# Optimization experiments

Measured on AMD Instinct MI355X. Metric: run time of the kernel, lower is better.

## Reference

```python
import jax, jax.numpy as jnp
import numpy as np

N_NODES = 100000


def _gcn_norm(edge_index, num_nodes):
    # PyG gcn_norm with add_self_loops=True, symmetric normalization.
    src = jnp.concatenate([edge_index[0], jnp.arange(num_nodes)])
    dst = jnp.concatenate([edge_index[1], jnp.arange(num_nodes)])
    ones = jnp.ones(src.shape[0], dtype=jnp.float32)
    deg = jax.ops.segment_sum(ones, dst, num_segments=num_nodes)
    dinv = jnp.where(deg > 0, jax.lax.rsqrt(deg), 0.0)
    norm = dinv[src] * dinv[dst]  # [E + N]
    return src, dst, norm


def _gcn_conv(x, W, b, src, dst, norm, num_nodes):
    h = x @ W                                  # dense transform first (PyG order)
    msg = h[src] * norm[:, None]               # gather + scale, [E+N, D]
    agg = jax.ops.segment_sum(msg, dst, num_segments=num_nodes)
    return agg + b


def setup_inputs() -> dict:
    key = jax.random.key(0)
    ks = jax.random.split(key, 6)
    F_in, D, C, E = 256, 64, 47, 1200000
    x = jax.random.normal(ks[0], (N_NODES, F_in), dtype=jnp.float32)
    edge_index = jax.random.randint(ks[1], (2, E), 0, N_NODES)
    W1 = jax.random.normal(ks[2], (F_in, D), dtype=jnp.float32) * (1.0 / np.sqrt(F_in))
    b1 = jnp.zeros((D,), dtype=jnp.float32)
    W2 = jax.random.normal(ks[3], (D, C), dtype=jnp.float32) * (1.0 / np.sqrt(D))
    b2 = jnp.zeros((C,), dtype=jnp.float32)
    return {"x": x, "edge_index": edge_index, "W1": W1, "b1": b1, "W2": W2, "b2": b2}


def reference(x, edge_index, W1, b1, W2, b2):
    src, dst, norm = _gcn_norm(edge_index, N_NODES)
    h = jax.nn.relu(_gcn_conv(x, W1, b1, src, dst, norm, N_NODES))
    # dropout: eval mode (training=False) -> identity
    out = _gcn_conv(h, W2, b2, src, dst, norm, N_NODES)
    return jax.nn.log_softmax(out, axis=1)
```

## Files before the change

### kernel.cpp

```cpp
#include <hip/hip_runtime.h>
#include <math.h>

#define NN 100000
#define FIN 256
#define D1 64
#define C2 47
#define S2 48
#define PREPB 76
#define NBKT 391
#define CAP 4096

typedef unsigned short u16;
typedef unsigned int u32;
typedef __attribute__((ext_vector_type(8))) short short8;
typedef __attribute__((ext_vector_type(4))) float floatx4;

__device__ __forceinline__ u16 f2b(float f) {
    union { float f; unsigned u; } v; v.f = f;
    unsigned r = v.u + 0x7FFF + ((v.u >> 16) & 1);
    return (u16)(r >> 16);
}
__device__ __forceinline__ float b2f_lo(u32 p) { union { unsigned u; float f; } v; v.u = p << 16; return v.f; }
__device__ __forceinline__ float b2f_hi(u32 p) { union { unsigned u; float f; } v; v.u = p & 0xFFFF0000u; return v.f; }

__global__ __launch_bounds__(256) void k_prep_bucket(
    const float* __restrict__ W1, const float* __restrict__ W2,
    u16* __restrict__ W1t, u16* __restrict__ W2t,
    const int* __restrict__ src, const int* __restrict__ dst, int E,
    int* __restrict__ bucketCnt, u32* __restrict__ ebuf)
{
    int b = blockIdx.x;
    if (b < PREPB) {
        int i = b * 256 + threadIdx.x;
        if (i < FIN * D1) {
            int c = i >> 8, k = i & 255;
            W1t[i] = f2b(W1[k * D1 + c]);
        } else if (i < FIN * D1 + D1 * S2) {
            int j = i - FIN * D1;
            int c = j >> 6, k = j & 63;
            W2t[j] = (c < C2) ? f2b(W2[k * C2 + c]) : (u16)0;
        }
        return;
    }
    __shared__ int hist[NBKT];
    __shared__ int base[NBKT];
    const int t = threadIdx.x;
    const int blk = b - PREPB;
    for (int i = t; i < NBKT; i += 256) hist[i] = 0;
    __syncthreads();

    int e0 = blk * 2048 + t;
    u32 pk[8]; int bk[8], tk[8];
    #pragma unroll
    for (int j = 0; j < 8; ++j) {
        int e = e0 + j * 256;
        bk[j] = -1;
        if (e < E) {
            int d = dst[e];
            int s = src[e];
            bk[j] = d >> 8;
            pk[j] = (u32)s | ((u32)(d & 255) << 17);
            tk[j] = atomicAdd(&hist[bk[j]], 1);
        }
    }
    __syncthreads();
    for (int i = t; i < NBKT; i += 256)
        base[i] = hist[i] ? atomicAdd(&bucketCnt[i], hist[i]) : 0;
    __syncthreads();
    #pragma unroll
    for (int j = 0; j < 8; ++j)
        if (bk[j] >= 0)
            ebuf[(size_t)bk[j] * CAP + base[bk[j]] + tk[j]] = pk[j];
}

__global__ __launch_bounds__(256) void k_csr_ptr(const int* __restrict__ bucketCnt,
                                                 const u32* __restrict__ ebuf,
                                                 int* __restrict__ rowptr,
                                                 float* __restrict__ dinv, int E) {
    __shared__ int sd[256];
    __shared__ int hist[256];
    const int b = blockIdx.x, t = threadIdx.x;
    int v = ((t < b) ? bucketCnt[t] : 0) + ((t + 256 < b) ? bucketCnt[t + 256] : 0);
    sd[t] = v; __syncthreads();
    for (int off = 128; off; off >>= 1) {
        if (t < off) sd[t] += sd[t + off];
        __syncthreads();
    }
    int ebase = sd[0];
    __syncthreads();

    hist[t] = 0;
    __syncthreads();
    const int cnt = bucketCnt[b];
    const u32* eb = ebuf + (size_t)b * CAP;
    for (int i = t; i < cnt; i += 256)
        atomicAdd(&hist[eb[i] >> 17], 1);
    __syncthreads();

    int h = hist[t];
    sd[t] = h; __syncthreads();
    for (int off = 1; off < 256; off <<= 1) {
        int u = (t >= off) ? sd[t - off] : 0;
        __syncthreads();
        sd[t] += u;
        __syncthreads();
    }
    int node = b * 256 + t;
    if (node <= NN) rowptr[node] = ebase + sd[t] - h;
    if (node < NN) dinv[node] = rsqrtf((float)h + 1.0f);
}

__global__ __launch_bounds__(256) void k_fill_gemm1(
    const int* __restrict__ bucketCnt, const u32* __restrict__ ebuf,
    const int* __restrict__ rowptr, int* __restrict__ colidx,
    const float* __restrict__ x, const u16* __restrict__ W1t,
    const float* __restrict__ dinv, u16* __restrict__ hs1)
{
    int b = blockIdx.x;
    const int t = threadIdx.x;
    if (b < NBKT) {
        __shared__ int cur[256];
        int node = b * 256 + t;
        cur[t] = (node < NN) ? rowptr[node] : 0;
        __syncthreads();
        const int cnt = bucketCnt[b];
        const u32* eb = ebuf + (size_t)b * CAP;
        for (int i = t; i < cnt; i += 256) {
            u32 p = eb[i];
            int pos = atomicAdd(&cur[p >> 17], 1);
            colidx[pos] = p & 0x1FFFF;
        }
        return;
    }
    __shared__ short As[2][64 * 40];
    __shared__ short Bs[2][64 * 40];
    const int bm = (b - NBKT) * 64;
    const int w = t >> 6, lane = t & 63;
    const int arow = t >> 2;
    const int ak0 = (t & 3) * 8;

    floatx4 acc[4] = {};
    const int gr = bm + arow;
    const bool rowok = gr < NN;
    const float* xrow = x + (size_t)(rowok ? gr : 0) * FIN + ak0;

    float4 v0 = make_float4(0.f,0.f,0.f,0.f), v1 = v0;
    if (rowok) { v0 = *(const float4*)(xrow); v1 = *(const float4*)(xrow + 4); }
    short8 wv = *(const short8*)(W1t + arow * FIN + ak0);
    {
        short8 av;
        av[0]=(short)f2b(v0.x); av[1]=(short)f2b(v0.y); av[2]=(short)f2b(v0.z); av[3]=(short)f2b(v0.w);
        av[4]=(short)f2b(v1.x); av[5]=(short)f2b(v1.y); av[6]=(short)f2b(v1.z); av[7]=(short)f2b(v1.w);
        *(short8*)(&As[0][arow * 40 + ak0]) = av;
        *(short8*)(&Bs[0][arow * 40 + ak0]) = wv;
    }
    __syncthreads();

    int cb_ = 0;
    for (int kt = 32; kt <= FIN; kt += 32) {
        const bool more = kt < FIN;
        float4 n0, n1; short8 nw;
        if (more) {
            if (rowok) { n0 = *(const float4*)(xrow + kt); n1 = *(const float4*)(xrow + kt + 4); }
            else { n0 = make_float4(0.f,0.f,0.f,0.f); n1 = n0; }
            nw = *(const short8*)(W1t + arow * FIN + kt + ak0);
        }
        short8 af = *(const short8*)(&As[cb_][(w * 16 + (lane & 15)) * 40 + (lane >> 4) * 8]);
        #pragma unroll
        for (int cb = 0; cb < 4; ++cb) {
            short8 bv = *(const short8*)(&Bs[cb_][(cb * 16 + (lane & 15)) * 40 + (lane >> 4) * 8]);
            acc[cb] = __builtin_amdgcn_mfma_f32_16x16x32_bf16(af, bv, acc[cb], 0, 0, 0);
        }
        if (!more) break;
        short8 av;
        av[0]=(short)f2b(n0.x); av[1]=(short)f2b(n0.y); av[2]=(short)f2b(n0.z); av[3]=(short)f2b(n0.w);
        av[4]=(short)f2b(n1.x); av[5]=(short)f2b(n1.y); av[6]=(short)f2b(n1.z); av[7]=(short)f2b(n1.w);
        *(short8*)(&As[cb_ ^ 1][arow * 40 + ak0]) = av;
        *(short8*)(&Bs[cb_ ^ 1][arow * 40 + ak0]) = nw;
        __syncthreads();
        cb_ ^= 1;
    }

    #pragma unroll
    for (int cb = 0; cb < 4; ++cb) {
        #pragma unroll
        for (int r = 0; r < 4; ++r) {
            int grow = bm + w * 16 + (lane >> 4) * 4 + r;
            if (grow < NN) {
                float v = acc[cb][r] * dinv[grow];
                hs1[(size_t)grow * D1 + cb * 16 + (lane & 15)] = f2b(v);
            }
        }
    }
}

__global__ __launch_bounds__(256) void k_gather_gemm2(
    const int* __restrict__ rowptr, const int* __restrict__ colidx,
    const float* __restrict__ dinv, const u16* __restrict__ hs1,
    const float* __restrict__ b1, const u16* __restrict__ W2t,
    u16* __restrict__ hs2)
{
    __shared__ short As[2][64 * 40];
    __shared__ short Bs[2][48 * 40];
    const int t = threadIdx.x;
    const int bm = blockIdx.x * 64;
    const int w = t >> 6;
    const int l32 = t & 31;

    for (int s = t; s < 384; s += 256) {
        int kt = s / 192, rem = s - kt * 192;
        int r = rem >> 2, j = rem & 3;
        *(short8*)(&Bs[kt][r * 40 + j * 8]) =
            *(const short8*)(W2t + r * D1 + kt * 32 + j * 8);
    }

    {
        const int g = (t >> 5) & 1;
        float2 bb = *(const float2*)(b1 + 2 * l32);
        const int kth = l32 >> 4;
        const int cs  = (2 * l32) & 31;
        #pragma unroll 1
        for (int i = 0; i < 8; ++i) {
            int rl = w * 16 + g * 8 + i;
            int node = bm + rl;
            if (node >= NN) break;
            int beg = rowptr[node], end = rowptr[node + 1];
            u32 pv = *((const u32*)(hs1 + (size_t)node * D1) + l32);
            float a0 = b2f_lo(pv), b0 = b2f_hi(pv);
            float a1 = 0.f, b1v = 0.f, a2 = 0.f, b2v = 0.f, a3 = 0.f, b3v = 0.f;
            int e = beg;
            for (; e + 8 <= end; e += 8) {
                int s0 = colidx[e+0], s1 = colidx[e+1], s2 = colidx[e+2], s3 = colidx[e+3];
                int s4 = colidx[e+4], s5 = colidx[e+5], s6 = colidx[e+6], s7 = colidx[e+7];
                u32 p0 = *((const u32*)(hs1 + (size_t)s0 * D1) + l32);
                u32 p1 = *((const u32*)(hs1 + (size_t)s1 * D1) + l32);
                u32 p2 = *((const u32*)(hs1 + (size_t)s2 * D1) + l32);
                u32 p3 = *((const u32*)(hs1 + (size_t)s3 * D1) + l32);
                u32 p4 = *((const u32*)(hs1 + (size_t)s4 * D1) + l32);
                u32 p5 = *((const u32*)(hs1 + (size_t)s5 * D1) + l32);
                u32 p6 = *((const u32*)(hs1 + (size_t)s6 * D1) + l32);
                u32 p7 = *((const u32*)(hs1 + (size_t)s7 * D1) + l32);
                a0 += b2f_lo(p0); b0  += b2f_hi(p0);
                a1 += b2f_lo(p1); b1v += b2f_hi(p1);
                a2 += b2f_lo(p2); b2v += b2f_hi(p2);
                a3 += b2f_lo(p3); b3v += b2f_hi(p3);
                a0 += b2f_lo(p4); b0  += b2f_hi(p4);
                a1 += b2f_lo(p5); b1v += b2f_hi(p5);
                a2 += b2f_lo(p6); b2v += b2f_hi(p6);
                a3 += b2f_lo(p7); b3v += b2f_hi(p7);
            }
            for (; e + 4 <= end; e += 4) {
                int s0 = colidx[e+0], s1 = colidx[e+1], s2 = colidx[e+2], s3 = colidx[e+3];
                u32 p0 = *((const u32*)(hs1 + (size_t)s0 * D1) + l32);
                u32 p1 = *((const u32*)(hs1 + (size_t)s1 * D1) + l32);
                u32 p2 = *((const u32*)(hs1 + (size_t)s2 * D1) + l32);
                u32 p3 = *((const u32*)(hs1 + (size_t)s3 * D1) + l32);
                a0 += b2f_lo(p0); b0  += b2f_hi(p0);
                a1 += b2f_lo(p1); b1v += b2f_hi(p1);
                a2 += b2f_lo(p2); b2v += b2f_hi(p2);
                a3 += b2f_lo(p3); b3v += b2f_hi(p3);
            }
            for (; e < end; ++e) {
                u32 p0 = *((const u32*)(hs1 + (size_t)colidx[e] * D1) + l32);
                a0 += b2f_lo(p0); b0 += b2f_hi(p0);
            }
            float dd = dinv[node];
            float f0 = fmaxf(fmaf(dd, (a0 + a1) + (a2 + a3), bb.x), 0.f);
            float f1 = fmaxf(fmaf(dd, (b0 + b1v) + (b2v + b3v), bb.y), 0.f);
            u32 pk = (u32)f2b(f0) | ((u32)f2b(f1) << 16);
            *(u32*)(&As[kth][rl * 40 + cs]) = pk;
        }
    }
    __syncthreads();

    const int lane = t & 63;
    floatx4 acc[3] = {};
    #pragma unroll
    for (int kt = 0; kt < 2; ++kt) {
        short8 af = *(const short8*)(&As[kt][(w * 16 + (lane & 15)) * 40 + (lane >> 4) * 8]);
        #pragma unroll
        for (int cb = 0; cb < 3; ++cb) {
            short8 bv = *(const short8*)(&Bs[kt][(cb * 16 + (lane & 15)) * 40 + (lane >> 4) * 8]);
            acc[cb] = __builtin_amdgcn_mfma_f32_16x16x32_bf16(af, bv, acc[cb], 0, 0, 0);
        }
    }

    #pragma unroll
    for (int cb = 0; cb < 3; ++cb) {
        #pragma unroll
        for (int r = 0; r < 4; ++r) {
            int grow = bm + w * 16 + (lane >> 4) * 4 + r;
            if (grow < NN) {
                float v = acc[cb][r] * dinv[grow];
                hs2[(size_t)grow * S2 + cb * 16 + (lane & 15)] = f2b(v);
            }
        }
    }
}

__global__ __launch_bounds__(256) void k_gather47_sm(const int* __restrict__ rowptr,
                                                     const int* __restrict__ colidx,
                                                     const float* __restrict__ dinv,
                                                     const u16* __restrict__ hs,
                                                     const float* __restrict__ b2,
                                                     float* __restrict__ out) {
    int node = blockIdx.x * 8 + (threadIdx.x >> 5);
    int l32 = threadIdx.x & 31;
    if (node >= NN) return;
    bool act = l32 < 24;
    int ll = act ? l32 : 0;
    int f0 = 2 * ll, f1 = f0 + 1;
    int beg = rowptr[node], end = rowptr[node + 1];
    u32 pv = *((const u32*)(hs + (size_t)node * S2) + ll);
    float a0 = b2f_lo(pv), b0 = b2f_hi(pv);
    float a1 = 0.f, b1v = 0.f, a2 = 0.f, b2v = 0.f, a3 = 0.f, b3v = 0.f;
    int e = beg;
    for (; e + 8 <= end; e += 8) {
        int s0 = colidx[e+0], s1 = colidx[e+1], s2 = colidx[e+2], s3 = colidx[e+3];
        int s4 = colidx[e+4], s5 = colidx[e+5], s6 = colidx[e+6], s7 = colidx[e+7];
        u32 p0 = *((const u32*)(hs + (size_t)s0 * S2) + ll);
        u32 p1 = *((const u32*)(hs + (size_t)s1 * S2) + ll);
        u32 p2 = *((const u32*)(hs + (size_t)s2 * S2) + ll);
        u32 p3 = *((const u32*)(hs + (size_t)s3 * S2) + ll);
        u32 p4 = *((const u32*)(hs + (size_t)s4 * S2) + ll);
        u32 p5 = *((const u32*)(hs + (size_t)s5 * S2) + ll);
        u32 p6 = *((const u32*)(hs + (size_t)s6 * S2) + ll);
        u32 p7 = *((const u32*)(hs + (size_t)s7 * S2) + ll);
        a0 += b2f_lo(p0); b0  += b2f_hi(p0);
        a1 += b2f_lo(p1); b1v += b2f_hi(p1);
        a2 += b2f_lo(p2); b2v += b2f_hi(p2);
        a3 += b2f_lo(p3); b3v += b2f_hi(p3);
        a0 += b2f_lo(p4); b0  += b2f_hi(p4);
        a1 += b2f_lo(p5); b1v += b2f_hi(p5);
        a2 += b2f_lo(p6); b2v += b2f_hi(p6);
        a3 += b2f_lo(p7); b3v += b2f_hi(p7);
    }
    for (; e + 4 <= end; e += 4) {
        int s0 = colidx[e+0], s1 = colidx[e+1], s2 = colidx[e+2], s3 = colidx[e+3];
        u32 p0 = *((const u32*)(hs + (size_t)s0 * S2) + ll);
        u32 p1 = *((const u32*)(hs + (size_t)s1 * S2) + ll);
        u32 p2 = *((const u32*)(hs + (size_t)s2 * S2) + ll);
        u32 p3 = *((const u32*)(hs + (size_t)s3 * S2) + ll);
        a0 += b2f_lo(p0); b0  += b2f_hi(p0);
        a1 += b2f_lo(p1); b1v += b2f_hi(p1);
        a2 += b2f_lo(p2); b2v += b2f_hi(p2);
        a3 += b2f_lo(p3); b3v += b2f_hi(p3);
    }
    for (; e < end; ++e) {
        u32 p0 = *((const u32*)(hs + (size_t)colidx[e] * S2) + ll);
        a0 += b2f_lo(p0); b0 += b2f_hi(p0);
    }
    float dd = dinv[node];
    float val0 = fmaf(dd, (a0 + a1) + (a2 + a3), b2[f0]);
    float val1 = (f1 < C2) ? fmaf(dd, (b0 + b1v) + (b2v + b3v), b2[f1]) : -INFINITY;

    float m = act ? fmaxf(val0, val1) : -INFINITY;
    #pragma unroll
    for (int off = 16; off; off >>= 1) m = fmaxf(m, __shfl_xor(m, off));
    float ex = act ? (expf(val0 - m) + ((f1 < C2) ? expf(val1 - m) : 0.f)) : 0.f;
    #pragma unroll
    for (int off = 16; off; off >>= 1) ex += __shfl_xor(ex, off);
    float ls = m + logf(ex);
    if (act) {
        out[(size_t)node * C2 + f0] = val0 - ls;
        if (f1 < C2) out[(size_t)node * C2 + f1] = val1 - ls;
    }
}

extern "C" void kernel_launch(void* const* d_in, const int* in_sizes, int n_in,
                              void* d_out, int out_size, void* d_ws, size_t ws_size,
                              hipStream_t stream) {
    const float* x  = (const float*)d_in[0];
    const int*   ei = (const int*)d_in[1];
    const float* W1 = (const float*)d_in[2];
    const float* b1 = (const float*)d_in[3];
    const float* W2 = (const float*)d_in[4];
    const float* b2 = (const float*)d_in[5];
    float* out = (float*)d_out;

    const int E = in_sizes[1] / 2;
    const int* src = ei;
    const int* dst = ei + E;

    char* ws = (char*)d_ws;
    float* dinv      = (float*)(ws);
    int*   bucketCnt = (int*)(ws + 0x80000);
    int*   rowptr    = (int*)(ws + 0x100000);
    u16*   W1t       = (u16*)(ws + 0x180000);
    u16*   W2t       = (u16*)(ws + 0x189000);
    u32*   ebuf      = (u32*)(ws + 0x200000);
    int*   colidx    = (int*)(ws + 0x900000);
    u16*   hs1       = (u16*)(ws + 0xE00000);
    u16*   hs2       = (u16*)(ws + 0x1B00000);

    const int nBk1 = (E + 2047) / 2048;
    const int gb1  = (NN + 63) / 64;

    hipMemsetAsync(bucketCnt, 0, NBKT * sizeof(int), stream);
    k_prep_bucket<<<PREPB + nBk1, 256, 0, stream>>>(W1, W2, W1t, W2t, src, dst, E,
                                                    bucketCnt, ebuf);
    k_csr_ptr<<<NBKT, 256, 0, stream>>>(bucketCnt, ebuf, rowptr, dinv, E);
    k_fill_gemm1<<<NBKT + gb1, 256, 0, stream>>>(bucketCnt, ebuf, rowptr, colidx,
                                                 x, W1t, dinv, hs1);
    k_gather_gemm2<<<gb1, 256, 0, stream>>>(rowptr, colidx, dinv, hs1, b1, W2t, hs2);
    k_gather47_sm<<<(NN + 7) / 8, 256, 0, stream>>>(rowptr, colidx, dinv, hs2, b2, out);
}
```

Before: 143.1 us.

## Fuse CSR pointer build into fill+GEMM1 kernel and widen gather lanes

Merges the rowptr/dinv computation into the colidx fill blocks of the GEMM1 kernel, which removes one launch. Because dinv is no longer ready when GEMM1 runs, the source-side dinv scaling moves into the layer-1 gather, at the cost of one extra dinv load per edge. Both gather kernels now use 16 lanes per node with 8-byte loads, so each wave covers more nodes. The edge bucketing kernel handles 4096 edges per block instead of 2048.

```diff
diff --git a/kernel.cpp b/kernel.cpp
--- a/kernel.cpp
+++ b/kernel.cpp
@@ -9,6 +9,7 @@
 #define PREPB 76
 #define NBKT 391
 #define CAP 4096
+#define EPB 4096
 
 typedef unsigned short u16;
 typedef unsigned int u32;
@@ -49,17 +50,16 @@
     for (int i = t; i < NBKT; i += 256) hist[i] = 0;
     __syncthreads();
 
-    int e0 = blk * 2048 + t;
-    u32 pk[8]; int bk[8], tk[8];
-    #pragma unroll
-    for (int j = 0; j < 8; ++j) {
+    int e0 = blk * EPB + t;
+    u32 pk[16]; int bk[16], tk[16];
+    #pragma unroll
+    for (int j = 0; j < 16; ++j) {
         int e = e0 + j * 256;
         bk[j] = -1;
         if (e < E) {
             int d = dst[e];
-            int s = src[e];
             bk[j] = d >> 8;
-            pk[j] = (u32)s | ((u32)(d & 255) << 17);
+            pk[j] = (u32)src[e] | ((u32)(d & 255) << 17);
             tk[j] = atomicAdd(&hist[bk[j]], 1);
         }
     }
@@ -68,63 +68,57 @@
         base[i] = hist[i] ? atomicAdd(&bucketCnt[i], hist[i]) : 0;
     __syncthreads();
     #pragma unroll
-    for (int j = 0; j < 8; ++j)
+    for (int j = 0; j < 16; ++j)
         if (bk[j] >= 0)
             ebuf[(size_t)bk[j] * CAP + base[bk[j]] + tk[j]] = pk[j];
 }
 
-__global__ __launch_bounds__(256) void k_csr_ptr(const int* __restrict__ bucketCnt,
-                                                 const u32* __restrict__ ebuf,
-                                                 int* __restrict__ rowptr,
-                                                 float* __restrict__ dinv, int E) {
-    __shared__ int sd[256];
-    __shared__ int hist[256];
-    const int b = blockIdx.x, t = threadIdx.x;
-    int v = ((t < b) ? bucketCnt[t] : 0) + ((t + 256 < b) ? bucketCnt[t + 256] : 0);
-    sd[t] = v; __syncthreads();
-    for (int off = 128; off; off >>= 1) {
-        if (t < off) sd[t] += sd[t + off];
-        __syncthreads();
-    }
-    int ebase = sd[0];
-    __syncthreads();
-
-    hist[t] = 0;
-    __syncthreads();
-    const int cnt = bucketCnt[b];
-    const u32* eb = ebuf + (size_t)b * CAP;
-    for (int i = t; i < cnt; i += 256)
-        atomicAdd(&hist[eb[i] >> 17], 1);
-    __syncthreads();
-
-    int h = hist[t];
-    sd[t] = h; __syncthreads();
-    for (int off = 1; off < 256; off <<= 1) {
-        int u = (t >= off) ? sd[t - off] : 0;
-        __syncthreads();
-        sd[t] += u;
-        __syncthreads();
-    }
-    int node = b * 256 + t;
-    if (node <= NN) rowptr[node] = ebase + sd[t] - h;
-    if (node < NN) dinv[node] = rsqrtf((float)h + 1.0f);
-}
-
-__global__ __launch_bounds__(256) void k_fill_gemm1(
+__global__ __launch_bounds__(256) void k_csrfill_gemm1(
     const int* __restrict__ bucketCnt, const u32* __restrict__ ebuf,
-    const int* __restrict__ rowptr, int* __restrict__ colidx,
+    int* __restrict__ rowptr, float* __restrict__ dinv, int* __restrict__ colidx,
     const float* __restrict__ x, const u16* __restrict__ W1t,
-    const float* __restrict__ dinv, u16* __restrict__ hs1)
+    u16* __restrict__ h1b, int E)
 {
+    __shared__ short As[2][64 * 40];
+    __shared__ short Bs[2][64 * 40];
     int b = blockIdx.x;
     const int t = threadIdx.x;
     if (b < NBKT) {
-        __shared__ int cur[256];
-        int node = b * 256 + t;
-        cur[t] = (node < NN) ? rowptr[node] : 0;
+        int* sd   = (int*)&As[0][0];
+        int* hist = sd + 256;
+        int* cur  = hist + 256;
+        int v = ((t < b) ? bucketCnt[t] : 0) + ((t + 256 < b) ? bucketCnt[t + 256] : 0);
+        sd[t] = v; __syncthreads();
+        for (int off = 128; off; off >>= 1) {
+            if (t < off) sd[t] += sd[t + off];
+            __syncthreads();
+        }
+        int ebase = sd[0];
+        __syncthreads();
+
+        hist[t] = 0;
         __syncthreads();
         const int cnt = bucketCnt[b];
         const u32* eb = ebuf + (size_t)b * CAP;
+        for (int i = t; i < cnt; i += 256)
+            atomicAdd(&hist[eb[i] >> 17], 1);
+        __syncthreads();
+
+        int h = hist[t];
+        sd[t] = h; __syncthreads();
+        for (int off = 1; off < 256; off <<= 1) {
+            int u = (t >= off) ? sd[t - off] : 0;
+            __syncthreads();
+            sd[t] += u;
+            __syncthreads();
+        }
+        int start = ebase + sd[t] - h;
+        int node = b * 256 + t;
+        if (node <= NN) rowptr[node] = start;
+        if (node < NN) dinv[node] = rsqrtf((float)h + 1.0f);
+        cur[t] = start;
+        __syncthreads();
+
         for (int i = t; i < cnt; i += 256) {
             u32 p = eb[i];
             int pos = atomicAdd(&cur[p >> 17], 1);
@@ -132,8 +126,6 @@
         }
         return;
     }
-    __shared__ short As[2][64 * 40];
-    __shared__ short Bs[2][64 * 40];
     const int bm = (b - NBKT) * 64;
     const int w = t >> 6, lane = t & 63;
     const int arow = t >> 2;
@@ -186,17 +178,15 @@
         #pragma unroll
         for (int r = 0; r < 4; ++r) {
             int grow = bm + w * 16 + (lane >> 4) * 4 + r;
-            if (grow < NN) {
-                float v = acc[cb][r] * dinv[grow];
-                hs1[(size_t)grow * D1 + cb * 16 + (lane & 15)] = f2b(v);
-            }
+            if (grow < NN)
+                h1b[(size_t)grow * D1 + cb * 16 + (lane & 15)] = f2b(acc[cb][r]);
         }
     }
 }
 
 __global__ __launch_bounds__(256) void k_gather_gemm2(
     const int* __restrict__ rowptr, const int* __restrict__ colidx,
-    const float* __restrict__ dinv, const u16* __restrict__ hs1,
+    const float* __restrict__ dinv, const u16* __restrict__ h1b,
     const float* __restrict__ b1, const u16* __restrict__ W2t,
     u16* __restrict__ hs2)
 {
@@ -205,7 +195,8 @@
     const int t = threadIdx.x;
     const int bm = blockIdx.x * 64;
     const int w = t >> 6;
-    const int l32 = t & 31;
+    const int g16 = (t >> 4) & 3;
+    const int l16 = t & 15;
 
     for (int s = t; s < 384; s += 256) {
         int kt = s / 192, rem = s - kt * 192;
@@ -215,60 +206,61 @@
     }
 
     {
-        const int g = (t >> 5) & 1;
-        float2 bb = *(const float2*)(b1 + 2 * l32);
-        const int kth = l32 >> 4;
-        const int cs  = (2 * l32) & 31;
+        float4 bb = *(const float4*)(b1 + 4 * l16);
+        const int col = 4 * l16;
+        const int kth = col >> 5;
+        const int cs  = col & 31;
         #pragma unroll 1
-        for (int i = 0; i < 8; ++i) {
-            int rl = w * 16 + g * 8 + i;
+        for (int i = 0; i < 4; ++i) {
+            int rl = w * 16 + g16 * 4 + i;
             int node = bm + rl;
             if (node >= NN) break;
             int beg = rowptr[node], end = rowptr[node + 1];
-            u32 pv = *((const u32*)(hs1 + (size_t)node * D1) + l32);
-            float a0 = b2f_lo(pv), b0 = b2f_hi(pv);
-            float a1 = 0.f, b1v = 0.f, a2 = 0.f, b2v = 0.f, a3 = 0.f, b3v = 0.f;
+            float dd = dinv[node];
+            uint2 sp = *((const uint2*)(h1b + (size_t)node * D1) + l16);
+            float ac[4][4];
+            ac[0][0] = dd * b2f_lo(sp.x); ac[0][1] = dd * b2f_hi(sp.x);
+            ac[0][2] = dd * b2f_lo(sp.y); ac[0][3] = dd * b2f_hi(sp.y);
+            #pragma unroll
+            for (int st = 1; st < 4; ++st)
+                ac[st][0] = ac[st][1] = ac[st][2] = ac[st][3] = 0.f;
             int e = beg;
             for (; e + 8 <= end; e += 8) {
-                int s0 = colidx[e+0], s1 = colidx[e+1], s2 = colidx[e+2], s3 = colidx[e+3];
-                int s4 = colidx[e+4], s5 = colidx[e+5], s6 = colidx[e+6], s7 = colidx[e+7];
-                u32 p0 = *((const u32*)(hs1 + (size_t)s0 * D1) + l32);
-                u32 p1 = *((const u32*)(hs1 + (size_t)s1 * D1) + l32);
-                u32 p2 = *((const u32*)(hs1 + (size_t)s2 * D1) + l32);
-                u32 p3 = *((const u32*)(hs1 + (size_t)s3 * D1) + l32);
-                u32 p4 = *((const u32*)(hs1 + (size_t)s4 * D1) + l32);
-                u32 p5 = *((const u32*)(hs1 + (size_t)s5 * D1) + l32);
-                u32 p6 = *((const u32*)(hs1 + (size_t)s6 * D1) + l32);
-                u32 p7 = *((const u32*)(hs1 + (size_t)s7 * D1) + l32);
-                a0 += b2f_lo(p0); b0  += b2f_hi(p0);
-                a1 += b2f_lo(p1); b1v += b2f_hi(p1);
-                a2 += b2f_lo(p2); b2v += b2f_hi(p2);
-                a3 += b2f_lo(p3); b3v += b2f_hi(p3);
-                a0 += b2f_lo(p4); b0  += b2f_hi(p4);
-                a1 += b2f_lo(p5); b1v += b2f_hi(p5);
-                a2 += b2f_lo(p6); b2v += b2f_hi(p6);
-                a3 += b2f_lo(p7); b3v += b2f_hi(p7);
-            }
-            for (; e + 4 <= end; e += 4) {
-                int s0 = colidx[e+0], s1 = colidx[e+1], s2 = colidx[e+2], s3 = colidx[e+3];
-                u32 p0 = *((const u32*)(hs1 + (size_t)s0 * D1) + l32);
-                u32 p1 = *((const u32*)(hs1 + (size_t)s1 * D1) + l32);
-                u32 p2 = *((const u32*)(hs1 + (size_t)s2 * D1) + l32);
-                u32 p3 = *((const u32*)(hs1 + (size_t)s3 * D1) + l32);
-                a0 += b2f_lo(p0); b0  += b2f_hi(p0);
-                a1 += b2f_lo(p1); b1v += b2f_hi(p1);
-                a2 += b2f_lo(p2); b2v += b2f_hi(p2);
-                a3 += b2f_lo(p3); b3v += b2f_hi(p3);
+                int c[8]; float ds[8]; uint2 p[8];
+                #pragma unroll
+                for (int j = 0; j < 8; ++j) c[j] = colidx[e + j];
+                #pragma unroll
+                for (int j = 0; j < 8; ++j) ds[j] = dinv[c[j]];
+                #pragma unroll
+                for (int j = 0; j < 8; ++j)
+                    p[j] = *((const uint2*)(h1b + (size_t)c[j] * D1) + l16);
+                #pragma unroll
+                for (int j = 0; j < 8; ++j) {
+                    ac[j & 3][0] += ds[j] * b2f_lo(p[j].x);
+                    ac[j & 3][1] += ds[j] * b2f_hi(p[j].x);
+                    ac[j & 3][2] += ds[j] * b2f_lo(p[j].y);
+                    ac[j & 3][3] += ds[j] * b2f_hi(p[j].y);
+                }
             }
             for (; e < end; ++e) {
-                u32 p0 = *((const u32*)(hs1 + (size_t)colidx[e] * D1) + l32);
-                a0 += b2f_lo(p0); b0 += b2f_hi(p0);
+                int c0 = colidx[e];
+                float d0 = dinv[c0];
+                uint2 p0 = *((const uint2*)(h1b + (size_t)c0 * D1) + l16);
+                ac[0][0] += d0 * b2f_lo(p0.x); ac[0][1] += d0 * b2f_hi(p0.x);
+                ac[0][2] += d0 * b2f_lo(p0.y); ac[0][3] += d0 * b2f_hi(p0.y);
             }
-            float dd = dinv[node];
-            float f0 = fmaxf(fmaf(dd, (a0 + a1) + (a2 + a3), bb.x), 0.f);
-            float f1 = fmaxf(fmaf(dd, (b0 + b1v) + (b2v + b3v), bb.y), 0.f);
-            u32 pk = (u32)f2b(f0) | ((u32)f2b(f1) << 16);
-            *(u32*)(&As[kth][rl * 40 + cs]) = pk;
+            float fv0 = (ac[0][0] + ac[1][0]) + (ac[2][0] + ac[3][0]);
+            float fv1 = (ac[0][1] + ac[1][1]) + (ac[2][1] + ac[3][1]);
+            float fv2 = (ac[0][2] + ac[1][2]) + (ac[2][2] + ac[3][2]);
+            float fv3 = (ac[0][3] + ac[1][3]) + (ac[2][3] + ac[3][3]);
+            float r0 = fmaxf(fmaf(dd, fv0, bb.x), 0.f);
+            float r1 = fmaxf(fmaf(dd, fv1, bb.y), 0.f);
+            float r2 = fmaxf(fmaf(dd, fv2, bb.z), 0.f);
+            float r3 = fmaxf(fmaf(dd, fv3, bb.w), 0.f);
+            u32 lo = (u32)f2b(r0) | ((u32)f2b(r1) << 16);
+            u32 hi = (u32)f2b(r2) | ((u32)f2b(r3) << 16);
+            *(u32*)(&As[kth][rl * 40 + cs]) = lo;
+            *(u32*)(&As[kth][rl * 40 + cs + 2]) = hi;
         }
     }
     __syncthreads();
@@ -304,66 +296,64 @@
                                                      const u16* __restrict__ hs,
                                                      const float* __restrict__ b2,
                                                      float* __restrict__ out) {
-    int node = blockIdx.x * 8 + (threadIdx.x >> 5);
-    int l32 = threadIdx.x & 31;
+    int node = blockIdx.x * 16 + (threadIdx.x >> 4);
+    int l16 = threadIdx.x & 15;
     if (node >= NN) return;
-    bool act = l32 < 24;
-    int ll = act ? l32 : 0;
-    int f0 = 2 * ll, f1 = f0 + 1;
+    bool act = l16 < 12;
+    int lc = act ? l16 : 0;
     int beg = rowptr[node], end = rowptr[node + 1];
-    u32 pv = *((const u32*)(hs + (size_t)node * S2) + ll);
-    float a0 = b2f_lo(pv), b0 = b2f_hi(pv);
-    float a1 = 0.f, b1v = 0.f, a2 = 0.f, b2v = 0.f, a3 = 0.f, b3v = 0.f;
+    uint2 sp = *((const uint2*)(hs + (size_t)node * S2) + lc);
+    float ac[4][4];
+    ac[0][0] = b2f_lo(sp.x); ac[0][1] = b2f_hi(sp.x);
+    ac[0][2] = b2f_lo(sp.y); ac[0][3] = b2f_hi(sp.y);
+    #pragma unroll
+    for (int st = 1; st < 4; ++st)
+        ac[st][0] = ac[st][1] = ac[st][2] = ac[st][3] = 0.f;
     int e = beg;
     for (; e + 8 <= end; e += 8) {
-        int s0 = colidx[e+0], s1 = colidx[e+1], s2 = colidx[e+2], s3 = colidx[e+3];
-        int s4 = colidx[e+4], s5 = colidx[e+5], s6 = colidx[e+6], s7 = colidx[e+7];
-        u32 p0 = *((const u32*)(hs + (size_t)s0 * S2) + ll);
-        u32 p1 = *((const u32*)(hs + (size_t)s1 * S2) + ll);
-        u32 p2 = *((const u32*)(hs + (size_t)s2 * S2) + ll);
-        u32 p3 = *((const u32*)(hs + (size_t)s3 * S2) + ll);
-        u32 p4 = *((const u32*)(hs + (size_t)s4 * S2) + ll);
-        u32 p5 = *((const u32*)(hs + (size_t)s5 * S2) + ll);
-        u32 p6 = *((const u32*)(hs + (size_t)s6 * S2) + ll);
-        u32 p7 = *((const u32*)(hs + (size_t)s7 * S2) + ll);
-        a0 += b2f_lo(p0); b0  += b2f_hi(p0);
-        a1 += b2f_lo(p1); b1v += b2f_hi(p1);
-        a2 += b2f_lo(p2); b2v += b2f_hi(p2);
-        a3 += b2f_lo(p3); b3v += b2f_hi(p3);
-        a0 += b2f_lo(p4); b0  += b2f_hi(p4);
-        a1 += b2f_lo(p5); b1v += b2f_hi(p5);
-        a2 += b2f_lo(p6); b2v += b2f_hi(p6);
-        a3 += b2f_lo(p7); b3v += b2f_hi(p7);
-    }
-    for (; e + 4 <= end; e += 4) {
-        int s0 = colidx[e+0], s1 = colidx[e+1], s2 = colidx[e+2], s3 = colidx[e+3];
-        u32 p0 = *((const u32*)(hs + (size_t)s0 * S2) + ll);
-        u32 p1 = *((const u32*)(hs + (size_t)s1 * S2) + ll);
-        u32 p2 = *((const u32*)(hs + (size_t)s2 * S2) + ll);
-        u32 p3 = *((const u32*)(hs + (size_t)s3 * S2) + ll);
-        a0 += b2f_lo(p0); b0  += b2f_hi(p0);
-        a1 += b2f_lo(p1); b1v += b2f_hi(p1);
-        a2 += b2f_lo(p2); b2v += b2f_hi(p2);
-        a3 += b2f_lo(p3); b3v += b2f_hi(p3);
+        int c[8]; uint2 p[8];
+        #pragma unroll
+        for (int j = 0; j < 8; ++j) c[j] = colidx[e + j];
+        #pragma unroll
+        for (int j = 0; j < 8; ++j)
+            p[j] = *((const uint2*)(hs + (size_t)c[j] * S2) + lc);
+        #pragma unroll
+        for (int j = 0; j < 8; ++j) {
+            ac[j & 3][0] += b2f_lo(p[j].x);
+            ac[j & 3][1] += b2f_hi(p[j].x);
+            ac[j & 3][2] += b2f_lo(p[j].y);
+            ac[j & 3][3] += b2f_hi(p[j].y);
+        }
     }
     for (; e < end; ++e) {
-        u32 p0 = *((const u32*)(hs + (size_t)colidx[e] * S2) + ll);
-        a0 += b2f_lo(p0); b0 += b2f_hi(p0);
+        uint2 p0 = *((const uint2*)(hs + (size_t)colidx[e] * S2) + lc);
+        ac[0][0] += b2f_lo(p0.x); ac[0][1] += b2f_hi(p0.x);
+        ac[0][2] += b2f_lo(p0.y); ac[0][3] += b2f_hi(p0.y);
     }
     float dd = dinv[node];
-    float val0 = fmaf(dd, (a0 + a1) + (a2 + a3), b2[f0]);
-    float val1 = (f1 < C2) ? fmaf(dd, (b0 + b1v) + (b2v + b3v), b2[f1]) : -INFINITY;
-
-    float m = act ? fmaxf(val0, val1) : -INFINITY;
-    #pragma unroll
-    for (int off = 16; off; off >>= 1) m = fmaxf(m, __shfl_xor(m, off));
-    float ex = act ? (expf(val0 - m) + ((f1 < C2) ? expf(val1 - m) : 0.f)) : 0.f;
-    #pragma unroll
-    for (int off = 16; off; off >>= 1) ex += __shfl_xor(ex, off);
+    float val[4];
+    float m = -INFINITY;
+    #pragma unroll
+    for (int k = 0; k < 4; ++k) {
+        int fe = 4 * l16 + k;
+        float f = (ac[0][k] + ac[1][k]) + (ac[2][k] + ac[3][k]);
+        bool valid = act && (fe < C2);
+        val[k] = valid ? fmaf(dd, f, b2[valid ? fe : 0]) : -INFINITY;
+        m = fmaxf(m, val[k]);
+    }
+    #pragma unroll
+    for (int off = 1; off < 16; off <<= 1) m = fmaxf(m, __shfl_xor(m, off));
+    float ex = 0.f;
+    #pragma unroll
+    for (int k = 0; k < 4; ++k)
+        if (val[k] > -INFINITY) ex += expf(val[k] - m);
+    #pragma unroll
+    for (int off = 1; off < 16; off <<= 1) ex += __shfl_xor(ex, off);
     float ls = m + logf(ex);
-    if (act) {
-        out[(size_t)node * C2 + f0] = val0 - ls;
-        if (f1 < C2) out[(size_t)node * C2 + f1] = val1 - ls;
+    #pragma unroll
+    for (int k = 0; k < 4; ++k) {
+        int fe = 4 * l16 + k;
+        if (act && fe < C2) out[(size_t)node * C2 + fe] = val[k] - ls;
     }
 }
 
@@ -390,18 +380,17 @@
     u16*   W2t       = (u16*)(ws + 0x189000);
     u32*   ebuf      = (u32*)(ws + 0x200000);
     int*   colidx    = (int*)(ws + 0x900000);
-    u16*   hs1       = (u16*)(ws + 0xE00000);
+    u16*   h1b       = (u16*)(ws + 0xE00000);
     u16*   hs2       = (u16*)(ws + 0x1B00000);
 
-    const int nBk1 = (E + 2047) / 2048;
+    const int nBk1 = (E + EPB - 1) / EPB;
     const int gb1  = (NN + 63) / 64;
 
     hipMemsetAsync(bucketCnt, 0, NBKT * sizeof(int), stream);
     k_prep_bucket<<<PREPB + nBk1, 256, 0, stream>>>(W1, W2, W1t, W2t, src, dst, E,
                                                     bucketCnt, ebuf);
-    k_csr_ptr<<<NBKT, 256, 0, stream>>>(bucketCnt, ebuf, rowptr, dinv, E);
-    k_fill_gemm1<<<NBKT + gb1, 256, 0, stream>>>(bucketCnt, ebuf, rowptr, colidx,
-                                                 x, W1t, dinv, hs1);
-    k_gather_gemm2<<<gb1, 256, 0, stream>>>(rowptr, colidx, dinv, hs1, b1, W2t, hs2);
-    k_gather47_sm<<<(NN + 7) / 8, 256, 0, stream>>>(rowptr, colidx, dinv, hs2, b2, out);
-}
+    k_csrfill_gemm1<<<NBKT + gb1, 256, 0, stream>>>(bucketCnt, ebuf, rowptr, dinv,
+                                                    colidx, x, W1t, h1b, E);
+    k_gather_gemm2<<<gb1, 256, 0, stream>>>(rowptr, colidx, dinv, h1b, b1, W2t, hs2);
+    k_gather47_sm<<<(NN + 15) / 16, 256, 0, stream>>>(rowptr, colidx, dinv, hs2, b2, out);
+}
```

Measured after the change: 158.2 us. 10.5% more time.

## Widen gather loads to 16-byte per lane and double edges per bucketing block

Applied to the files above, without the earlier changes.

Both neighbor-gather kernels now assign 8 lanes per node, each loading a 16-byte uint4 (8 bf16 features), instead of 32 lanes loading 4 bytes each. This packs more nodes per wave and cuts the number of memory instructions per gathered row. The bucketing kernel handles 4096 edges per block instead of 2048, which reduces global atomics on bucketCnt. rowptr[NN] is now set explicitly to E. The trade-off is higher register pressure and fewer concurrent memory requests per node, and the shuffle reductions in the softmax are narrower.

```diff
diff --git a/kernel.cpp b/kernel.cpp
--- a/kernel.cpp
+++ b/kernel.cpp
@@ -9,6 +9,7 @@
 #define PREPB 76
 #define NBKT 391
 #define CAP 4096
+#define EPB 4096
 
 typedef unsigned short u16;
 typedef unsigned int u32;
@@ -49,17 +50,16 @@
     for (int i = t; i < NBKT; i += 256) hist[i] = 0;
     __syncthreads();
 
-    int e0 = blk * 2048 + t;
-    u32 pk[8]; int bk[8], tk[8];
-    #pragma unroll
-    for (int j = 0; j < 8; ++j) {
+    int e0 = blk * EPB + t;
+    u32 pk[16]; int bk[16], tk[16];
+    #pragma unroll
+    for (int j = 0; j < 16; ++j) {
         int e = e0 + j * 256;
         bk[j] = -1;
         if (e < E) {
             int d = dst[e];
-            int s = src[e];
             bk[j] = d >> 8;
-            pk[j] = (u32)s | ((u32)(d & 255) << 17);
+            pk[j] = (u32)src[e] | ((u32)(d & 255) << 17);
             tk[j] = atomicAdd(&hist[bk[j]], 1);
         }
     }
@@ -68,7 +68,7 @@
         base[i] = hist[i] ? atomicAdd(&bucketCnt[i], hist[i]) : 0;
     __syncthreads();
     #pragma unroll
-    for (int j = 0; j < 8; ++j)
+    for (int j = 0; j < 16; ++j)
         if (bk[j] >= 0)
             ebuf[(size_t)bk[j] * CAP + base[bk[j]] + tk[j]] = pk[j];
 }
@@ -108,6 +108,7 @@
     int node = b * 256 + t;
     if (node <= NN) rowptr[node] = ebase + sd[t] - h;
     if (node < NN) dinv[node] = rsqrtf((float)h + 1.0f);
+    if (b == 0 && t == 0) rowptr[NN] = E;
 }
 
 __global__ __launch_bounds__(256) void k_fill_gemm1(
@@ -205,7 +206,8 @@
     const int t = threadIdx.x;
     const int bm = blockIdx.x * 64;
     const int w = t >> 6;
-    const int l32 = t & 31;
+    const int g8 = (t >> 3) & 7;
+    const int l8 = t & 7;
 
     for (int s = t; s < 384; s += 256) {
         int kt = s / 192, rem = s - kt * 192;
@@ -215,60 +217,55 @@
     }
 
     {
-        const int g = (t >> 5) & 1;
-        float2 bb = *(const float2*)(b1 + 2 * l32);
-        const int kth = l32 >> 4;
-        const int cs  = (2 * l32) & 31;
+        const int col = 8 * l8;
+        const int kth = l8 >> 2;
+        const int cs  = col & 31;
+        float4 bbl = *(const float4*)(b1 + col);
+        float4 bbh = *(const float4*)(b1 + col + 4);
         #pragma unroll 1
-        for (int i = 0; i < 8; ++i) {
-            int rl = w * 16 + g * 8 + i;
+        for (int i = 0; i < 2; ++i) {
+            int rl = w * 16 + g8 * 2 + i;
             int node = bm + rl;
             if (node >= NN) break;
             int beg = rowptr[node], end = rowptr[node + 1];
-            u32 pv = *((const u32*)(hs1 + (size_t)node * D1) + l32);
-            float a0 = b2f_lo(pv), b0 = b2f_hi(pv);
-            float a1 = 0.f, b1v = 0.f, a2 = 0.f, b2v = 0.f, a3 = 0.f, b3v = 0.f;
+            uint4 sp = *((const uint4*)(hs1 + (size_t)node * D1) + l8);
+            float a0=b2f_lo(sp.x), a1=b2f_hi(sp.x), a2=b2f_lo(sp.y), a3=b2f_hi(sp.y);
+            float a4=b2f_lo(sp.z), a5=b2f_hi(sp.z), a6=b2f_lo(sp.w), a7=b2f_hi(sp.w);
+            float c0=0.f,c1=0.f,c2=0.f,c3=0.f,c4=0.f,c5=0.f,c6=0.f,c7=0.f;
             int e = beg;
-            for (; e + 8 <= end; e += 8) {
-                int s0 = colidx[e+0], s1 = colidx[e+1], s2 = colidx[e+2], s3 = colidx[e+3];
-                int s4 = colidx[e+4], s5 = colidx[e+5], s6 = colidx[e+6], s7 = colidx[e+7];
-                u32 p0 = *((const u32*)(hs1 + (size_t)s0 * D1) + l32);
-                u32 p1 = *((const u32*)(hs1 + (size_t)s1 * D1) + l32);
-                u32 p2 = *((const u32*)(hs1 + (size_t)s2 * D1) + l32);
-                u32 p3 = *((const u32*)(hs1 + (size_t)s3 * D1) + l32);
-                u32 p4 = *((const u32*)(hs1 + (size_t)s4 * D1) + l32);
-                u32 p5 = *((const u32*)(hs1 + (size_t)s5 * D1) + l32);
-                u32 p6 = *((const u32*)(hs1 + (size_t)s6 * D1) + l32);
-                u32 p7 = *((const u32*)(hs1 + (size_t)s7 * D1) + l32);
-                a0 += b2f_lo(p0); b0  += b2f_hi(p0);
-                a1 += b2f_lo(p1); b1v += b2f_hi(p1);
-                a2 += b2f_lo(p2); b2v += b2f_hi(p2);
-                a3 += b2f_lo(p3); b3v += b2f_hi(p3);
-                a0 += b2f_lo(p4); b0  += b2f_hi(p4);
-                a1 += b2f_lo(p5); b1v += b2f_hi(p5);
-                a2 += b2f_lo(p6); b2v += b2f_hi(p6);
-                a3 += b2f_lo(p7); b3v += b2f_hi(p7);
-            }
             for (; e + 4 <= end; e += 4) {
                 int s0 = colidx[e+0], s1 = colidx[e+1], s2 = colidx[e+2], s3 = colidx[e+3];
-                u32 p0 = *((const u32*)(hs1 + (size_t)s0 * D1) + l32);
-                u32 p1 = *((const u32*)(hs1 + (size_t)s1 * D1) + l32);
-                u32 p2 = *((const u32*)(hs1 + (size_t)s2 * D1) + l32);
-                u32 p3 = *((const u32*)(hs1 + (size_t)s3 * D1) + l32);
-                a0 += b2f_lo(p0); b0  += b2f_hi(p0);
-                a1 += b2f_lo(p1); b1v += b2f_hi(p1);
-                a2 += b2f_lo(p2); b2v += b2f_hi(p2);
-                a3 += b2f_lo(p3); b3v += b2f_hi(p3);
+                uint4 p0 = *((const uint4*)(hs1 + (size_t)s0 * D1) + l8);
+                uint4 p1 = *((const uint4*)(hs1 + (size_t)s1 * D1) + l8);
+                uint4 p2 = *((const uint4*)(hs1 + (size_t)s2 * D1) + l8);
+                uint4 p3 = *((const uint4*)(hs1 + (size_t)s3 * D1) + l8);
+                a0+=b2f_lo(p0.x); a1+=b2f_hi(p0.x); a2+=b2f_lo(p0.y); a3+=b2f_hi(p0.y);
+                a4+=b2f_lo(p0.z); a5+=b2f_hi(p0.z); a6+=b2f_lo(p0.w); a7+=b2f_hi(p0.w);
+                c0+=b2f_lo(p1.x); c1+=b2f_hi(p1.x); c2+=b2f_lo(p1.y); c3+=b2f_hi(p1.y);
+                c4+=b2f_lo(p1.z); c5+=b2f_hi(p1.z); c6+=b2f_lo(p1.w); c7+=b2f_hi(p1.w);
+                a0+=b2f_lo(p2.x); a1+=b2f_hi(p2.x); a2+=b2f_lo(p2.y); a3+=b2f_hi(p2.y);
+                a4+=b2f_lo(p2.z); a5+=b2f_hi(p2.z); a6+=b2f_lo(p2.w); a7+=b2f_hi(p2.w);
+                c0+=b2f_lo(p3.x); c1+=b2f_hi(p3.x); c2+=b2f_lo(p3.y); c3+=b2f_hi(p3.y);
+                c4+=b2f_lo(p3.z); c5+=b2f_hi(p3.z); c6+=b2f_lo(p3.w); c7+=b2f_hi(p3.w);
             }
             for (; e < end; ++e) {
-                u32 p0 = *((const u32*)(hs1 + (size_t)colidx[e] * D1) + l32);
-                a0 += b2f_lo(p0); b0 += b2f_hi(p0);
+                uint4 p0 = *((const uint4*)(hs1 + (size_t)colidx[e] * D1) + l8);
+                a0+=b2f_lo(p0.x); a1+=b2f_hi(p0.x); a2+=b2f_lo(p0.y); a3+=b2f_hi(p0.y);
+                a4+=b2f_lo(p0.z); a5+=b2f_hi(p0.z); a6+=b2f_lo(p0.w); a7+=b2f_hi(p0.w);
             }
             float dd = dinv[node];
-            float f0 = fmaxf(fmaf(dd, (a0 + a1) + (a2 + a3), bb.x), 0.f);
-            float f1 = fmaxf(fmaf(dd, (b0 + b1v) + (b2v + b3v), bb.y), 0.f);
-            u32 pk = (u32)f2b(f0) | ((u32)f2b(f1) << 16);
-            *(u32*)(&As[kth][rl * 40 + cs]) = pk;
+            float r0 = fmaxf(fmaf(dd, a0 + c0, bbl.x), 0.f);
+            float r1 = fmaxf(fmaf(dd, a1 + c1, bbl.y), 0.f);
+            float r2 = fmaxf(fmaf(dd, a2 + c2, bbl.z), 0.f);
+            float r3 = fmaxf(fmaf(dd, a3 + c3, bbl.w), 0.f);
+            float r4 = fmaxf(fmaf(dd, a4 + c4, bbh.x), 0.f);
+            float r5 = fmaxf(fmaf(dd, a5 + c5, bbh.y), 0.f);
+            float r6 = fmaxf(fmaf(dd, a6 + c6, bbh.z), 0.f);
+            float r7 = fmaxf(fmaf(dd, a7 + c7, bbh.w), 0.f);
+            short8 pk;
+            pk[0]=(short)f2b(r0); pk[1]=(short)f2b(r1); pk[2]=(short)f2b(r2); pk[3]=(short)f2b(r3);
+            pk[4]=(short)f2b(r4); pk[5]=(short)f2b(r5); pk[6]=(short)f2b(r6); pk[7]=(short)f2b(r7);
+            *(short8*)(&As[kth][rl * 40 + cs]) = pk;
         }
     }
     __syncthreads();
@@ -304,66 +301,62 @@
                                                      const u16* __restrict__ hs,
                                                      const float* __restrict__ b2,
                                                      float* __restrict__ out) {
-    int node = blockIdx.x * 8 + (threadIdx.x >> 5);
-    int l32 = threadIdx.x & 31;
+    int node = blockIdx.x * 32 + (threadIdx.x >> 3);
+    int l8 = threadIdx.x & 7;
     if (node >= NN) return;
-    bool act = l32 < 24;
-    int ll = act ? l32 : 0;
-    int f0 = 2 * ll, f1 = f0 + 1;
+    bool act = l8 < 6;
+    int lc = act ? l8 : 0;
     int beg = rowptr[node], end = rowptr[node + 1];
-    u32 pv = *((const u32*)(hs + (size_t)node * S2) + ll);
-    float a0 = b2f_lo(pv), b0 = b2f_hi(pv);
-    float a1 = 0.f, b1v = 0.f, a2 = 0.f, b2v = 0.f, a3 = 0.f, b3v = 0.f;
+    uint4 sp = *((const uint4*)(hs + (size_t)node * S2) + lc);
+    float a0=b2f_lo(sp.x), a1=b2f_hi(sp.x), a2=b2f_lo(sp.y), a3=b2f_hi(sp.y);
+    float a4=b2f_lo(sp.z), a5=b2f_hi(sp.z), a6=b2f_lo(sp.w), a7=b2f_hi(sp.w);
+    float c0=0.f,c1=0.f,c2=0.f,c3=0.f,c4=0.f,c5=0.f,c6=0.f,c7=0.f;
     int e = beg;
-    for (; e + 8 <= end; e += 8) {
-        int s0 = colidx[e+0], s1 = colidx[e+1], s2 = colidx[e+2], s3 = colidx[e+3];
-        int s4 = colidx[e+4], s5 = colidx[e+5], s6 = colidx[e+6], s7 = colidx[e+7];
-        u32 p0 = *((const u32*)(hs + (size_t)s0 * S2) + ll);
-        u32 p1 = *((const u32*)(hs + (size_t)s1 * S2) + ll);
-        u32 p2 = *((const u32*)(hs + (size_t)s2 * S2) + ll);
-        u32 p3 = *((const u32*)(hs + (size_t)s3 * S2) + ll);
-        u32 p4 = *((const u32*)(hs + (size_t)s4 * S2) + ll);
-        u32 p5 = *((const u32*)(hs + (size_t)s5 * S2) + ll);
-        u32 p6 = *((const u32*)(hs + (size_t)s6 * S2) + ll);
-        u32 p7 = *((const u32*)(hs + (size_t)s7 * S2) + ll);
-        a0 += b2f_lo(p0); b0  += b2f_hi(p0);
-        a1 += b2f_lo(p1); b1v += b2f_hi(p1);
-        a2 += b2f_lo(p2); b2v += b2f_hi(p2);
-        a3 += b2f_lo(p3); b3v += b2f_hi(p3);
-        a0 += b2f_lo(p4); b0  += b2f_hi(p4);
-        a1 += b2f_lo(p5); b1v += b2f_hi(p5);
-        a2 += b2f_lo(p6); b2v += b2f_hi(p6);
-        a3 += b2f_lo(p7); b3v += b2f_hi(p7);
-    }
     for (; e + 4 <= end; e += 4) {
         int s0 = colidx[e+0], s1 = colidx[e+1], s2 = colidx[e+2], s3 = colidx[e+3];
-        u32 p0 = *((const u32*)(hs + (size_t)s0 * S2) + ll);
-        u32 p1 = *((const u32*)(hs + (size_t)s1 * S2) + ll);
-        u32 p2 = *((const u32*)(hs + (size_t)s2 * S2) + ll);
-        u32 p3 = *((const u32*)(hs + (size_t)s3 * S2) + ll);
-        a0 += b2f_lo(p0); b0  += b2f_hi(p0);
-        a1 += b2f_lo(p1); b1v += b2f_hi(p1);
-        a2 += b2f_lo(p2); b2v += b2f_hi(p2);
-        a3 += b2f_lo(p3); b3v += b2f_hi(p3);
+        uint4 p0 = *((const uint4*)(hs + (size_t)s0 * S2) + lc);
+        uint4 p1 = *((const uint4*)(hs + (size_t)s1 * S2) + lc);
+        uint4 p2 = *((const uint4*)(hs + (size_t)s2 * S2) + lc);
+        uint4 p3 = *((const uint4*)(hs + (size_t)s3 * S2) + lc);
+        a0+=b2f_lo(p0.x); a1+=b2f_hi(p0.x); a2+=b2f_lo(p0.y); a3+=b2f_hi(p0.y);
+        a4+=b2f_lo(p0.z); a5+=b2f_hi(p0.z); a6+=b2f_lo(p0.w); a7+=b2f_hi(p0.w);
+        c0+=b2f_lo(p1.x); c1+=b2f_hi(p1.x); c2+=b2f_lo(p1.y); c3+=b2f_hi(p1.y);
+        c4+=b2f_lo(p1.z); c5+=b2f_hi(p1.z); c6+=b2f_lo(p1.w); c7+=b2f_hi(p1.w);
+        a0+=b2f_lo(p2.x); a1+=b2f_hi(p2.x); a2+=b2f_lo(p2.y); a3+=b2f_hi(p2.y);
+        a4+=b2f_lo(p2.z); a5+=b2f_hi(p2.z); a6+=b2f_lo(p2.w); a7+=b2f_hi(p2.w);
+        c0+=b2f_lo(p3.x); c1+=b2f_hi(p3.x); c2+=b2f_lo(p3.y); c3+=b2f_hi(p3.y);
+        c4+=b2f_lo(p3.z); c5+=b2f_hi(p3.z); c6+=b2f_lo(p3.w); c7+=b2f_hi(p3.w);
     }
     for (; e < end; ++e) {
-        u32 p0 = *((const u32*)(hs + (size_t)colidx[e] * S2) + ll);
-        a0 += b2f_lo(p0); b0 += b2f_hi(p0);
+        uint4 p0 = *((const uint4*)(hs + (size_t)colidx[e] * S2) + lc);
+        a0+=b2f_lo(p0.x); a1+=b2f_hi(p0.x); a2+=b2f_lo(p0.y); a3+=b2f_hi(p0.y);
+        a4+=b2f_lo(p0.z); a5+=b2f_hi(p0.z); a6+=b2f_lo(p0.w); a7+=b2f_hi(p0.w);
     }
     float dd = dinv[node];
-    float val0 = fmaf(dd, (a0 + a1) + (a2 + a3), b2[f0]);
-    float val1 = (f1 < C2) ? fmaf(dd, (b0 + b1v) + (b2v + b3v), b2[f1]) : -INFINITY;
-
-    float m = act ? fmaxf(val0, val1) : -INFINITY;
-    #pragma unroll
-    for (int off = 16; off; off >>= 1) m = fmaxf(m, __shfl_xor(m, off));
-    float ex = act ? (expf(val0 - m) + ((f1 < C2) ? expf(val1 - m) : 0.f)) : 0.f;
-    #pragma unroll
-    for (int off = 16; off; off >>= 1) ex += __shfl_xor(ex, off);
+    float fv[8] = { a0+c0, a1+c1, a2+c2, a3+c3, a4+c4, a5+c5, a6+c6, a7+c7 };
+    const int fb = 8 * lc;
+    float val[8];
+    float m = -INFINITY;
+    #pragma unroll
+    for (int k = 0; k < 8; ++k) {
+        int fe = fb + k;
+        bool valid = act && (fe < C2);
+        val[k] = valid ? fmaf(dd, fv[k], b2[valid ? fe : 0]) : -INFINITY;
+        m = fmaxf(m, val[k]);
+    }
+    #pragma unroll
+    for (int off = 1; off < 8; off <<= 1) m = fmaxf(m, __shfl_xor(m, off));
+    float ex = 0.f;
+    #pragma unroll
+    for (int k = 0; k < 8; ++k)
+        if (val[k] > -INFINITY) ex += expf(val[k] - m);
+    #pragma unroll
+    for (int off = 1; off < 8; off <<= 1) ex += __shfl_xor(ex, off);
     float ls = m + logf(ex);
-    if (act) {
-        out[(size_t)node * C2 + f0] = val0 - ls;
-        if (f1 < C2) out[(size_t)node * C2 + f1] = val1 - ls;
+    #pragma unroll
+    for (int k = 0; k < 8; ++k) {
+        int fe = fb + k;
+        if (act && fe < C2) out[(size_t)node * C2 + fe] = val[k] - ls;
     }
 }
 
@@ -393,7 +386,7 @@
     u16*   hs1       = (u16*)(ws + 0xE00000);
     u16*   hs2       = (u16*)(ws + 0x1B00000);
 
-    const int nBk1 = (E + 2047) / 2048;
+    const int nBk1 = (E + EPB - 1) / EPB;
     const int gb1  = (NN + 63) / 64;
 
     hipMemsetAsync(bucketCnt, 0, NBKT * sizeof(int), stream);
@@ -403,5 +396,5 @@
     k_fill_gemm1<<<NBKT + gb1, 256, 0, stream>>>(bucketCnt, ebuf, rowptr, colidx,
                                                  x, W1t, dinv, hs1);
     k_gather_gemm2<<<gb1, 256, 0, stream>>>(rowptr, colidx, dinv, hs1, b1, W2t, hs2);
-    k_gather47_sm<<<(NN + 7) / 8, 256, 0, stream>>>(rowptr, colidx, dinv, hs2, b2, out);
-}
+    k_gather47_sm<<<(NN + 31) / 32, 256, 0, stream>>>(rowptr, colidx, dinv, hs2, b2, out);
+}
```

After: 134.8 us. 5.8% less time.
